# Optimization experiments

Measured on AMD Instinct MI355X. Metric: run time of the kernel, lower is better.

Reference implementation:

```python
import jax, jax.numpy as jnp
import numpy as np

B, C, H, W = 2, 320, 64, 128
MAXDISP = 48
NUM_GROUPS = 40
R = 16  # channel-attention reduction ratio


def setup_inputs() -> dict:
    key = jax.random.key(0)
    k0, k1, k2, k3 = jax.random.split(key, 4)
    ref = jax.random.normal(k0, (B, C, H, W), jnp.float32)
    tgt = jax.random.normal(k1, (B, C, H, W), jnp.float32)
    # CMCAM channel-attention params: GAP -> FC(C->C/R) -> ReLU -> FC(C/R->C) -> sigmoid
    w1 = jax.random.normal(k2, (C // R, C), jnp.float32) * (1.0 / np.sqrt(C))
    b1 = jnp.zeros((C // R,), jnp.float32)
    w2 = jax.random.normal(k3, (C, C // R), jnp.float32) * (1.0 / np.sqrt(C // R))
    b2 = jnp.zeros((C,), jnp.float32)
    return {"refimg_fea": ref, "targetimg_fea": tgt, "w1": w1, "b1": b1, "w2": w2, "b2": b2}


def _cmcam_mask(x, w1, b1, w2, b2):
    # x: [B,C,H,W] -> mask [B,C,1,1] in (0,1)
    gap = x.mean(axis=(2, 3))                      # [B,C]
    h = jax.nn.relu(gap @ w1.T + b1)               # [B,C/R]
    m = jax.nn.sigmoid(h @ w2.T + b2)              # [B,C]
    return m[:, :, None, None]


def _build_gwc_volume(ref, tgt, maxdisp, num_groups):
    # groupwise correlation (mean over channels_per_group) at each disparity shift
    b, c, h, w = ref.shape
    cpg = c // num_groups
    rg = ref.reshape(b, num_groups, cpg, h, w)
    tg = tgt.reshape(b, num_groups, cpg, h, w)
    slices = []
    for d in range(maxdisp):  # fixed small structural loop
        if d == 0:
            cost = (rg * tg).mean(axis=2)                          # [B,G,H,W]
        else:
            cost = (rg[..., d:] * tg[..., : w - d]).mean(axis=2)   # [B,G,H,W-d]
            cost = jnp.pad(cost, ((0, 0), (0, 0), (0, 0), (d, 0)))
        slices.append(cost)
    return jnp.stack(slices, axis=2)  # [B,G,D,H,W]


def reference(refimg_fea, targetimg_fea, w1, b1, w2, b2):
    ref_mask = _cmcam_mask(refimg_fea, w1, b1, w2, b2)
    tg_mask = _cmcam_mask(targetimg_fea, w1, b1, w2, b2)
    ref_hf = refimg_fea * ref_mask
    ref_ctr = refimg_fea * (1.0 - ref_mask)
    tg_hf = targetimg_fea * tg_mask
    tg_ctr = targetimg_fea * (1.0 - tg_mask)
    corr_hf = _build_gwc_volume(ref_hf, tg_hf, MAXDISP, NUM_GROUPS)
    corr_ctr = _build_gwc_volume(ref_ctr, tg_ctr, MAXDISP, NUM_GROUPS)
    return jnp.concatenate([corr_hf, corr_ctr], axis=1)  # [B, 2G, D, H, W]
```

## Files before the change

### kernel.cpp

```cpp
#include <hip/hip_runtime.h>
#include <hip/hip_bf16.h>

#define BB 2
#define CC 320
#define HH 64
#define WW 128
#define MAXDISP 48
#define GG 40
#define CPG 8
#define CR 20

__global__ __launch_bounds__(256) void gap_kernel(
    const float* __restrict__ ref, const float* __restrict__ tgt,
    float* __restrict__ gap ) {
  int bid = blockIdx.x;
  int img = bid / (BB * CC);
  int rc  = bid - img * (BB * CC);
  const float* src = (img ? tgt : ref) + (size_t)rc * (HH * WW);
  const float4* v = reinterpret_cast<const float4*>(src);
  float acc = 0.f;
  for (int i = threadIdx.x; i < (HH * WW) / 4; i += 256) {
    float4 x = v[i];
    acc += (x.x + x.y) + (x.z + x.w);
  }
  for (int off = 32; off; off >>= 1) acc += __shfl_down(acc, off, 64);
  __shared__ float part[4];
  if ((threadIdx.x & 63) == 0) part[threadIdx.x >> 6] = acc;
  __syncthreads();
  if (threadIdx.x == 0) {
    float s = (part[0] + part[1]) + (part[2] + part[3]);
    gap[bid] = s * (1.0f / (HH * WW));
  }
}

__global__ __launch_bounds__(128) void mask_kernel(
    const float* __restrict__ gap,
    const float* __restrict__ w1, const float* __restrict__ b1,
    const float* __restrict__ w2, const float* __restrict__ b2,
    float* __restrict__ alpha, float* __restrict__ beta ) {
  __shared__ float gs[2 * BB * CC];
  __shared__ float hs[2 * BB * CR];
  __shared__ float ms[2 * BB * CC];
  int tid = threadIdx.x;
  for (int i = tid; i < 2 * BB * CC; i += 128) gs[i] = gap[i];
  __syncthreads();
  if (tid < 2 * BB * CR) {
    int j = tid % CR;
    int ib = tid / CR;
    float s = b1[j];
    const float* wrow = w1 + j * CC;
    const float* grow = gs + ib * CC;
    for (int c = 0; c < CC; ++c) s += wrow[c] * grow[c];
    hs[tid] = s > 0.f ? s : 0.f;
  }
  __syncthreads();
  for (int i = tid; i < 2 * BB * CC; i += 128) {
    int c = i % CC;
    int ib = i / CC;
    float s = b2[c];
    const float* hrow = hs + ib * CR;
    const float* wrow = w2 + c * CR;
#pragma unroll
    for (int j = 0; j < CR; ++j) s += wrow[j] * hrow[j];
    ms[i] = 1.f / (1.f + expf(-s));
  }
  __syncthreads();
  for (int i = tid; i < BB * CC; i += 128) {
    float mr = ms[i];
    float mt = ms[BB * CC + i];
    alpha[i] = mr * mt * 0.125f;
    beta[i]  = (1.f - mr) * (1.f - mt) * 0.125f;
  }
}

__global__ __launch_bounds__(256) void volume_kernel(
    const float* __restrict__ ref, const float* __restrict__ tgt,
    const float* __restrict__ alpha, const float* __restrict__ beta,
    float* __restrict__ out) {
  __shared__ float Tl[2][CPG][WW];
  const int H2 = HH / 2;
  int bid = blockIdx.x;
  int b   = bid / (GG * H2);
  int rem = bid - b * (GG * H2);
  int g   = rem / H2;
  int h2  = rem - g * H2;
  int tid = threadIdx.x;
  int hl  = tid >> 7;
  int w   = tid & 127;
  int h   = h2 * 2 + hl;

  size_t base = ((size_t)(b * CC + g * CPG) * HH + h) * WW + w;
  float rf[CPG];
#pragma unroll
  for (int c = 0; c < CPG; ++c) {
    rf[c] = ref[base + (size_t)c * (HH * WW)];
    Tl[hl][c][w] = tgt[base + (size_t)c * (HH * WW)];
  }
  float al[CPG], be[CPG];
#pragma unroll
  for (int c = 0; c < CPG; ++c) {
    al[c] = alpha[b * CC + g * CPG + c];
    be[c] = beta[b * CC + g * CPG + c];
  }
  __syncthreads();

  size_t out_hf = (((size_t)(b * 2 * GG + g) * MAXDISP) * HH + h) * WW + w;
  size_t out_ct = out_hf + (size_t)GG * MAXDISP * HH * WW;
#pragma unroll 4
  for (int d = 0; d < MAXDISP; ++d) {
    int wd = w - d;
    float mask = wd >= 0 ? 1.0f : 0.0f;
    int wc = wd >= 0 ? wd : 0;
    float shf = 0.f, sct = 0.f;
#pragma unroll
    for (int c = 0; c < CPG; ++c) {
      float p = rf[c] * Tl[hl][c][wc];
      shf += p * al[c];
      sct += p * be[c];
    }
    out[out_hf] = shf * mask;
    out[out_ct] = sct * mask;
    out_hf += HH * WW;
    out_ct += HH * WW;
  }
}

extern "C" void kernel_launch(void* const* d_in, const int* in_sizes, int n_in,
                              void* d_out, int out_size, void* d_ws, size_t ws_size,
                              hipStream_t stream) {
  const float* ref = (const float*)d_in[0];
  const float* tgt = (const float*)d_in[1];
  const float* w1  = (const float*)d_in[2];
  const float* b1  = (const float*)d_in[3];
  const float* w2  = (const float*)d_in[4];
  const float* b2  = (const float*)d_in[5];
  float* out = (float*)d_out;

  float* ws    = (float*)d_ws;
  float* gap   = ws;
  float* alpha = ws + 1280;
  float* beta  = ws + 1920;

  gap_kernel<<<2 * BB * CC, 256, 0, stream>>>(ref, tgt, gap);
  mask_kernel<<<1, 128, 0, stream>>>(gap, w1, b1, w2, b2, alpha, beta);
  volume_kernel<<<BB * GG * (HH / 2), 256, 0, stream>>>(ref, tgt, alpha, beta, out);
}
```

Measured before the change: 75.64 us.

## Restructure volume kernel to compute 4 pixels per thread with disparity slots and float4 stores

After: 65.60 us. 13.3% less time.

```diff
diff --git a/kernel.cpp b/kernel.cpp
--- a/kernel.cpp
+++ b/kernel.cpp
@@ -9,6 +9,8 @@
 #define GG 40
 #define CPG 8
 #define CR 20
+
+typedef float fx4 __attribute__((ext_vector_type(4)));
 
 __global__ __launch_bounds__(256) void gap_kernel(
     const float* __restrict__ ref, const float* __restrict__ tgt,
@@ -33,7 +35,7 @@
   }
 }
 
-__global__ __launch_bounds__(128) void mask_kernel(
+__global__ __launch_bounds__(256) void mask_kernel(
     const float* __restrict__ gap,
     const float* __restrict__ w1, const float* __restrict__ b1,
     const float* __restrict__ w2, const float* __restrict__ b2,
@@ -42,19 +44,28 @@
   __shared__ float hs[2 * BB * CR];
   __shared__ float ms[2 * BB * CC];
   int tid = threadIdx.x;
-  for (int i = tid; i < 2 * BB * CC; i += 128) gs[i] = gap[i];
-  __syncthreads();
-  if (tid < 2 * BB * CR) {
-    int j = tid % CR;
-    int ib = tid / CR;
-    float s = b1[j];
-    const float* wrow = w1 + j * CC;
-    const float* grow = gs + ib * CC;
-    for (int c = 0; c < CC; ++c) s += wrow[c] * grow[c];
-    hs[tid] = s > 0.f ? s : 0.f;
-  }
-  __syncthreads();
-  for (int i = tid; i < 2 * BB * CC; i += 128) {
+  for (int i = tid; i < 2 * BB * CC; i += 256) gs[i] = gap[i];
+  __syncthreads();
+  if (tid < 2 * 2 * BB * CR) {
+    int p = tid >> 1, half = tid & 1;
+    int j = p % CR;
+    int ib = p / CR;
+    const float4* wrow = reinterpret_cast<const float4*>(w1 + j * CC);
+    const float4* grow = reinterpret_cast<const float4*>(gs + ib * CC);
+    float s = 0.f;
+#pragma unroll 5
+    for (int c = half * 40; c < half * 40 + 40; ++c) {
+      float4 a = wrow[c], g = grow[c];
+      s += a.x * g.x + a.y * g.y + a.z * g.z + a.w * g.w;
+    }
+    s += __shfl_xor(s, 1, 64);
+    if (!half) {
+      s += b1[j];
+      hs[p] = s > 0.f ? s : 0.f;
+    }
+  }
+  __syncthreads();
+  for (int i = tid; i < 2 * BB * CC; i += 256) {
     int c = i % CC;
     int ib = i / CC;
     float s = b2[c];
@@ -65,7 +76,7 @@
     ms[i] = 1.f / (1.f + expf(-s));
   }
   __syncthreads();
-  for (int i = tid; i < BB * CC; i += 128) {
+  for (int i = tid; i < BB * CC; i += 256) {
     float mr = ms[i];
     float mt = ms[BB * CC + i];
     alpha[i] = mr * mt * 0.125f;
@@ -78,50 +89,94 @@
     const float* __restrict__ alpha, const float* __restrict__ beta,
     float* __restrict__ out) {
   __shared__ float Tl[2][CPG][WW];
-  const int H2 = HH / 2;
   int bid = blockIdx.x;
-  int b   = bid / (GG * H2);
-  int rem = bid - b * (GG * H2);
-  int g   = rem / H2;
-  int h2  = rem - g * H2;
+  int b   = bid / (GG * 32);
+  int rem = bid - b * (GG * 32);
+  int g   = rem >> 5;
+  int h2  = rem & 31;
   int tid = threadIdx.x;
-  int hl  = tid >> 7;
-  int w   = tid & 127;
-  int h   = h2 * 2 + hl;
-
-  size_t base = ((size_t)(b * CC + g * CPG) * HH + h) * WW + w;
-  float rf[CPG];
+  int dslot = tid >> 6;
+  int hl    = (tid >> 5) & 1;
+  int w4    = tid & 31;
+  int wq    = w4 << 2;
+  int d0    = dslot * 12;
+  int h     = h2 * 2 + hl;
+
+  {
+    int c_s = tid >> 5;
+    int xq  = (tid & 31) << 2;
+    int k   = (xq >> 5) & 3;
+    size_t tb = ((size_t)((b * CC + g * CPG + c_s) * HH) + h2 * 2) * WW + xq;
+    float4 v0 = *reinterpret_cast<const float4*>(tgt + tb);
+    float4 v1 = *reinterpret_cast<const float4*>(tgt + tb + WW);
+    float4 q0 = (k & 1) ? make_float4(v0.y, v0.x, v0.w, v0.z) : v0;
+    q0 = (k & 2) ? make_float4(q0.z, q0.w, q0.x, q0.y) : q0;
+    float4 q1 = (k & 1) ? make_float4(v1.y, v1.x, v1.w, v1.z) : v1;
+    q1 = (k & 2) ? make_float4(q1.z, q1.w, q1.x, q1.y) : q1;
+    *reinterpret_cast<float4*>(&Tl[0][c_s][xq]) = q0;
+    *reinterpret_cast<float4*>(&Tl[1][c_s][xq]) = q1;
+  }
+
+  float rf[CPG][4];
+  float al[CPG], be[CPG];
+  size_t rbase = ((size_t)((b * CC + g * CPG) * HH) + h) * WW + wq;
 #pragma unroll
   for (int c = 0; c < CPG; ++c) {
-    rf[c] = ref[base + (size_t)c * (HH * WW)];
-    Tl[hl][c][w] = tgt[base + (size_t)c * (HH * WW)];
-  }
-  float al[CPG], be[CPG];
-#pragma unroll
-  for (int c = 0; c < CPG; ++c) {
+    float4 rv = *reinterpret_cast<const float4*>(ref + rbase + (size_t)c * (HH * WW));
+    rf[c][0] = rv.x; rf[c][1] = rv.y; rf[c][2] = rv.z; rf[c][3] = rv.w;
     al[c] = alpha[b * CC + g * CPG + c];
     be[c] = beta[b * CC + g * CPG + c];
   }
   __syncthreads();
 
-  size_t out_hf = (((size_t)(b * 2 * GG + g) * MAXDISP) * HH + h) * WW + w;
-  size_t out_ct = out_hf + (size_t)GG * MAXDISP * HH * WW;
-#pragma unroll 4
-  for (int d = 0; d < MAXDISP; ++d) {
-    int wd = w - d;
-    float mask = wd >= 0 ? 1.0f : 0.0f;
-    int wc = wd >= 0 ? wd : 0;
-    float shf = 0.f, sct = 0.f;
+  const int A = wq - d0;
+  float t[CPG][4];
+#pragma unroll
+  for (int r = 0; r < 4; ++r) {
+    int x  = A + r;
+    int xc = x < 0 ? 0 : x;
+    int xs = xc ^ ((xc >> 5) & 3);
 #pragma unroll
     for (int c = 0; c < CPG; ++c) {
-      float p = rf[c] * Tl[hl][c][wc];
-      shf += p * al[c];
-      sct += p * be[c];
-    }
-    out[out_hf] = shf * mask;
-    out[out_ct] = sct * mask;
-    out_hf += HH * WW;
-    out_ct += HH * WW;
+      float v = Tl[hl][c][xs];
+      t[c][r] = x < 0 ? 0.f : v;
+    }
+  }
+
+  size_t o_hf = (((size_t)(b * 2 * GG + g) * MAXDISP + d0) * HH + h) * WW + wq;
+  size_t o_ct = o_hf + (size_t)GG * MAXDISP * HH * WW;
+#pragma unroll
+  for (int i = 0; i < 12; ++i) {
+    if (i > 0) {
+      int x  = A - i;
+      int xc = x < 0 ? 0 : x;
+      int xs = xc ^ ((xc >> 5) & 3);
+      const int s = (16 - i) & 3;
+#pragma unroll
+      for (int c = 0; c < CPG; ++c) {
+        float v = Tl[hl][c][xs];
+        t[c][s] = x < 0 ? 0.f : v;
+      }
+    }
+    float o0h = 0.f, o1h = 0.f, o2h = 0.f, o3h = 0.f;
+    float o0c = 0.f, o1c = 0.f, o2c = 0.f, o3c = 0.f;
+#pragma unroll
+    for (int c = 0; c < CPG; ++c) {
+      float p0 = rf[c][0] * t[c][(16 + 0 - i) & 3];
+      float p1 = rf[c][1] * t[c][(16 + 1 - i) & 3];
+      float p2 = rf[c][2] * t[c][(16 + 2 - i) & 3];
+      float p3 = rf[c][3] * t[c][(16 + 3 - i) & 3];
+      o0h += p0 * al[c]; o0c += p0 * be[c];
+      o1h += p1 * al[c]; o1c += p1 * be[c];
+      o2h += p2 * al[c]; o2c += p2 * be[c];
+      o3h += p3 * al[c]; o3c += p3 * be[c];
+    }
+    fx4 vh = {o0h, o1h, o2h, o3h};
+    fx4 vc = {o0c, o1c, o2c, o3c};
+    __builtin_nontemporal_store(vh, reinterpret_cast<fx4*>(out + o_hf));
+    __builtin_nontemporal_store(vc, reinterpret_cast<fx4*>(out + o_ct));
+    o_hf += HH * WW;
+    o_ct += HH * WW;
   }
 }
 
@@ -142,6 +197,6 @@
   float* beta  = ws + 1920;
 
   gap_kernel<<<2 * BB * CC, 256, 0, stream>>>(ref, tgt, gap);
-  mask_kernel<<<1, 128, 0, stream>>>(gap, w1, b1, w2, b2, alpha, beta);
-  volume_kernel<<<BB * GG * (HH / 2), 256, 0, stream>>>(ref, tgt, alpha, beta, out);
-}
+  mask_kernel<<<1, 256, 0, stream>>>(gap, w1, b1, w2, b2, alpha, beta);
+  volume_kernel<<<BB * GG * 32, 256, 0, stream>>>(ref, tgt, alpha, beta, out);
+}
```
